# Optimization experiments

Measured on AMD Instinct MI355X. Metric: run time of the kernel, lower is better.

Reference implementation:

```python
import jax, jax.numpy as jnp
import numpy as np

N = 50000      # nodes
E = 800000     # edges
G = 64         # graphs in batch
H = 256        # hidden_channels
CE = 128       # coord embed dim = H//2
OTH = 6        # in_channels - 3
ED = 8         # edge_dim
EE = 128       # edge_embedding_dim
GD = 16        # global_dim
L = 3          # num_layers


def setup_inputs() -> dict:
    key = jax.random.key(0)
    ks = jax.random.split(key, 24)
    s = 0.05
    inp = {
        "x": jax.random.normal(ks[0], (N, 9), jnp.float32),
        "edge_index": jax.random.randint(ks[1], (2, E), 0, N),
        "batch": jnp.sort(jax.random.randint(ks[2], (N,), 0, G)),
        "edge_attr": jax.random.normal(ks[3], (E, ED), jnp.float32),
        "global_x": jax.random.normal(ks[4], (G, GD), jnp.float32),
        # coordinate embedder (Linear 3->128 + relu)
        "coord_W": jax.random.normal(ks[5], (3, CE), jnp.float32) * s,
        "coord_b": jnp.zeros((CE,), jnp.float32),
        # node_mlp (Linear 6->128 + relu)
        "node_W": jax.random.normal(ks[6], (OTH, CE), jnp.float32) * s,
        "node_b": jnp.zeros((CE,), jnp.float32),
        # edge processor (Linear 8->128 + relu) and projection 128->256
        "edge_W": jax.random.normal(ks[7], (ED, EE), jnp.float32) * s,
        "edge_b": jnp.zeros((EE,), jnp.float32),
        "proj_W": jax.random.normal(ks[8], (EE, H), jnp.float32) * s,
        "proj_b": jnp.zeros((H,), jnp.float32),
        # stacked GCN layer weights
        "gcn_W": jax.random.normal(ks[9], (L, H, H), jnp.float32) * s,
        "gcn_b": jnp.zeros((L, H), jnp.float32),
        # attention pooling
        "attn_w": jax.random.normal(ks[10], (H,), jnp.float32) * s,
        "attn_b": jnp.zeros((), jnp.float32),
        # global_mlp: Linear 16->256, relu, Linear 256->256
        "gmlp_W1": jax.random.normal(ks[11], (GD, H), jnp.float32) * s,
        "gmlp_b1": jnp.zeros((H,), jnp.float32),
        "gmlp_W2": jax.random.normal(ks[12], (H, H), jnp.float32) * s,
        "gmlp_b2": jnp.zeros((H,), jnp.float32),
        # fc_out: Linear 512->256, relu, Linear 256->1
        "fc_W1": jax.random.normal(ks[13], (2 * H, H), jnp.float32) * s,
        "fc_b1": jnp.zeros((H,), jnp.float32),
        "fc_W2": jax.random.normal(ks[14], (H, 1), jnp.float32) * s,
        "fc_b2": jnp.zeros((1,), jnp.float32),
    }
    return inp


def _segsum(v, idx, num):
    return jax.ops.segment_sum(v, idx, num_segments=num)


def reference(x, edge_index, batch, edge_attr, global_x,
              coord_W, coord_b, node_W, node_b, edge_W, edge_b,
              proj_W, proj_b, gcn_W, gcn_b, attn_w, attn_b,
              gmlp_W1, gmlp_b1, gmlp_W2, gmlp_b2,
              fc_W1, fc_b1, fc_W2, fc_b2):
    relu = jax.nn.relu
    # --- node embedding: coords + other features ---
    coord_emb = relu(x[:, :3] @ coord_W + coord_b)          # [N, 128]
    other_emb = relu(x[:, 3:] @ node_W + node_b)            # [N, 128]
    x_emb = jnp.concatenate([coord_emb, other_emb], axis=1)  # [N, 256]

    # --- edge embedding, aggregated to target nodes (index_add over col) ---
    edge_emb = relu(edge_attr @ edge_W + edge_b) @ proj_W + proj_b  # [E, 256]
    col0 = edge_index[1]
    node_msg = _segsum(edge_emb, col0, N)                    # [N, 256]

    # --- GCN normalization with self-loops ---
    sl = jnp.arange(N)
    row = jnp.concatenate([edge_index[0], sl])
    col = jnp.concatenate([edge_index[1], sl])
    deg = _segsum(jnp.ones_like(col, jnp.float32), col, N)   # >= 1
    dnorm = jax.lax.rsqrt(deg)
    efac = (dnorm[row] * dnorm[col])[:, None]                # [E+N, 1]

    # --- stacked GCN layers (edge messages re-added each layer, per source) ---
    for i in range(L):
        x_in = x_emb + node_msg
        h = x_in @ gcn_W[i]                                  # [N, 256]
        x_emb = _segsum(h[row] * efac, col, N) + gcn_b[i]
        if i < L - 1:
            x_emb = relu(x_emb)

    # --- attention pooling (per-graph softmax over batch index) ---
    scores = x_emb @ attn_w + attn_b                         # [N]
    m = jax.ops.segment_max(scores, batch, num_segments=G)
    e = jnp.exp(scores - m[batch])
    denom = _segsum(e, batch, G)
    attn = e / denom[batch]
    graph_emb = _segsum(x_emb * attn[:, None], batch, G)     # [G, 256]

    # --- global features + head ---
    g = relu(global_x @ gmlp_W1 + gmlp_b1) @ gmlp_W2 + gmlp_b2
    hcat = jnp.concatenate([graph_emb, g], axis=-1)          # [G, 512]
    out = relu(hcat @ fc_W1 + fc_b1) @ fc_W2 + fc_b2         # [G, 1]
    return out
```

## Files before the change

kernel.cpp:

```cpp
#include <hip/hip_runtime.h>


typedef float f32x4 __attribute__((ext_vector_type(4)));
typedef short s16x8 __attribute__((ext_vector_type(8)));

__device__ __forceinline__ unsigned short f2bf(float f) {
  union { float f; unsigned u; } v{f};
  unsigned r = v.u + 0x7fff + ((v.u >> 16) & 1);
  return (unsigned short)(r >> 16);
}
__device__ __forceinline__ float bf2f(unsigned short s) {
  union { unsigned u; float f; } v{(unsigned)s << 16};
  return v.f;
}
__device__ __forceinline__ float blo(unsigned u) {
  union { unsigned x; float f; } v{u << 16};
  return v.f;
}
__device__ __forceinline__ float bhi(unsigned u) {
  union { unsigned x; float f; } v{u & 0xffff0000u};
  return v.f;
}
__device__ __forceinline__ unsigned pk2(float a, float b) {
  return (unsigned)f2bf(a) | ((unsigned)f2bf(b) << 16);
}

__global__ void node_embed_kernel(const float* __restrict__ x,
                                  const float* __restrict__ coord_W, const float* __restrict__ coord_b,
                                  const float* __restrict__ node_W, const float* __restrict__ node_b,
                                  short* __restrict__ x0, int N) {
  int tid = threadIdx.x;
  int node = blockIdx.x * 8 + (tid >> 5);
  if (node >= N) return;
  int ch0 = (tid & 31) * 8;
  const float* xr = x + (size_t)node * 9;
  float a[8];
  if (ch0 < 128) {
    float4 b0 = *(const float4*)&coord_b[ch0];
    float4 b1 = *(const float4*)&coord_b[ch0 + 4];
    a[0]=b0.x; a[1]=b0.y; a[2]=b0.z; a[3]=b0.w; a[4]=b1.x; a[5]=b1.y; a[6]=b1.z; a[7]=b1.w;
#pragma unroll
    for (int k = 0; k < 3; k++) {
      float xv = xr[k];
      float4 w0 = *(const float4*)&coord_W[k * 128 + ch0];
      float4 w1 = *(const float4*)&coord_W[k * 128 + ch0 + 4];
      a[0] = fmaf(xv, w0.x, a[0]); a[1] = fmaf(xv, w0.y, a[1]);
      a[2] = fmaf(xv, w0.z, a[2]); a[3] = fmaf(xv, w0.w, a[3]);
      a[4] = fmaf(xv, w1.x, a[4]); a[5] = fmaf(xv, w1.y, a[5]);
      a[6] = fmaf(xv, w1.z, a[6]); a[7] = fmaf(xv, w1.w, a[7]);
    }
  } else {
    int c0 = ch0 - 128;
    float4 b0 = *(const float4*)&node_b[c0];
    float4 b1 = *(const float4*)&node_b[c0 + 4];
    a[0]=b0.x; a[1]=b0.y; a[2]=b0.z; a[3]=b0.w; a[4]=b1.x; a[5]=b1.y; a[6]=b1.z; a[7]=b1.w;
#pragma unroll
    for (int k = 0; k < 6; k++) {
      float xv = xr[3 + k];
      float4 w0 = *(const float4*)&node_W[k * 128 + c0];
      float4 w1 = *(const float4*)&node_W[k * 128 + c0 + 4];
      a[0] = fmaf(xv, w0.x, a[0]); a[1] = fmaf(xv, w0.y, a[1]);
      a[2] = fmaf(xv, w0.z, a[2]); a[3] = fmaf(xv, w0.w, a[3]);
      a[4] = fmaf(xv, w1.x, a[4]); a[5] = fmaf(xv, w1.y, a[5]);
      a[6] = fmaf(xv, w1.z, a[6]); a[7] = fmaf(xv, w1.w, a[7]);
    }
  }
  uint4 o;
  o.x = pk2(fmaxf(a[0], 0.f), fmaxf(a[1], 0.f));
  o.y = pk2(fmaxf(a[2], 0.f), fmaxf(a[3], 0.f));
  o.z = pk2(fmaxf(a[4], 0.f), fmaxf(a[5], 0.f));
  o.w = pk2(fmaxf(a[6], 0.f), fmaxf(a[7], 0.f));
  *(uint4*)&x0[(size_t)node * 256 + ch0] = o;
}

__global__ void count_kernel(const int* __restrict__ col, int* __restrict__ cnt, int E) {
  int e = blockIdx.x * 256 + threadIdx.x;
  if (e < E) atomicAdd(&cnt[col[e]], 1);
}

__global__ void breduce_kernel(const int* __restrict__ cnt, int* __restrict__ partials, int N) {
  __shared__ int red[256];
  int t = threadIdx.x;
  int i = blockIdx.x * 256 + t;
  int v = (i < N) ? cnt[i] : 0;
  red[t] = v;
  __syncthreads();
  for (int off = 128; off; off >>= 1) {
    if (t < off) red[t] += red[t + off];
    __syncthreads();
  }
  if (t == 0) partials[blockIdx.x] = red[0];
}

__global__ void scan_partials_kernel(int* __restrict__ partials, int nb) {
  __shared__ int s[1024];
  int t = threadIdx.x;
  for (int i = t; i < nb; i += 256) s[i] = partials[i];
  __syncthreads();
  if (t == 0) {
    int run = 0;
    for (int i = 0; i < nb; i++) { int c = s[i]; s[i] = run; run += c; }
  }
  __syncthreads();
  for (int i = t; i < nb; i += 256) partials[i] = s[i];
}

__global__ void scan_apply_kernel(const int* __restrict__ cnt, const int* __restrict__ partials,
                                  int* __restrict__ rowstart, float* __restrict__ dnorm,
                                  int* __restrict__ cursor, int N) {
  __shared__ int red[256];
  int t = threadIdx.x;
  int i = blockIdx.x * 256 + t;
  int v = (i < N) ? cnt[i] : 0;
  red[t] = v;
  __syncthreads();
  for (int off = 1; off < 256; off <<= 1) {
    int x = (t >= off) ? red[t - off] : 0;
    __syncthreads();
    red[t] += x;
    __syncthreads();
  }
  if (i < N) {
    int ex = red[t] - v + partials[blockIdx.x];
    rowstart[i] = ex;
    dnorm[i] = rsqrtf((float)(v + 1));
    cursor[i] = 0;
    if (i == N - 1) rowstart[N] = ex + v;
  }
}

__global__ void scatter_kernel(const int* __restrict__ row, const int* __restrict__ col,
                               const int* __restrict__ rowstart, int* __restrict__ cursor,
                               const float* __restrict__ dnorm,
                               int4* __restrict__ pk, int E) {
  int e = blockIdx.x * 256 + threadIdx.x;
  if (e >= E) return;
  int c = col[e], r = row[e];
  int p = atomicAdd(&cursor[c], 1);
  int slot = rowstart[c] + p;
  pk[slot] = make_int4(e, r, __float_as_int(dnorm[r] * dnorm[c]), 0);
}

__global__ void wt_kernel(const float* __restrict__ gcn_W, const float* __restrict__ proj_W,
                          short* __restrict__ gcnWt, short* __restrict__ projWt) {
  int idx = blockIdx.x * 256 + threadIdx.x;
  if (idx < 3 * 65536) {
    int l = idx >> 16, r = idx & 65535, n = r >> 8, k = r & 255;
    gcnWt[idx] = (short)f2bf(gcn_W[l * 65536 + k * 256 + n]);
  } else {
    int j = idx - 3 * 65536;
    int n = j >> 7, k = j & 127;
    projWt[j] = (short)f2bf(proj_W[k * 256 + n]);
  }
}

__global__ void edge_msg_kernel(const float* __restrict__ edge_attr,
                                const int4* __restrict__ pk,
                                const int* __restrict__ rowstart,
                                const float* __restrict__ edge_W, const float* __restrict__ edge_b,
                                short* __restrict__ msg128, int N) {
  int node = blockIdx.x;
  int ch = threadIdx.x;
  __shared__ float sW[8 * 128];
  __shared__ float sb[128];
  for (int i = ch; i < 8 * 128; i += 128) sW[i] = edge_W[i];
  sb[ch] = edge_b[ch];
  __syncthreads();
  float acc = 0.f;
  int s0 = rowstart[node], s1 = rowstart[node + 1];
  for (int s = s0; s < s1; s++) {
    int eid = pk[s].x;
    const float4* ea = (const float4*)(edge_attr + (size_t)eid * 8);
    float4 e0 = ea[0], e1 = ea[1];
    float t = sb[ch];
    t = fmaf(e0.x, sW[0 * 128 + ch], t);
    t = fmaf(e0.y, sW[1 * 128 + ch], t);
    t = fmaf(e0.z, sW[2 * 128 + ch], t);
    t = fmaf(e0.w, sW[3 * 128 + ch], t);
    t = fmaf(e1.x, sW[4 * 128 + ch], t);
    t = fmaf(e1.y, sW[5 * 128 + ch], t);
    t = fmaf(e1.z, sW[6 * 128 + ch], t);
    t = fmaf(e1.w, sW[7 * 128 + ch], t);
    acc += fmaxf(t, 0.f);
  }
  msg128[(size_t)node * 128 + ch] = (short)f2bf(acc);
}

__global__ void __launch_bounds__(256) fused_proj_gemm(
    const short* __restrict__ msg128, const short* __restrict__ projWt,
    const float* __restrict__ proj_b, const int* __restrict__ cnt,
    const short* __restrict__ x0, const short* __restrict__ W0t,
    short* __restrict__ node_msg, short* __restrict__ hout, int N) {
  __shared__ short As[64][136];
  __shared__ short Xs[64][264];
  int tid = threadIdx.x;
  int n0 = blockIdx.x * 64;
  for (int i = tid; i < 64 * 32; i += 256) {
    int r = i >> 5, c4 = (i & 31) << 2;
    int n = n0 + r;
    uint2 v = make_uint2(0, 0);
    if (n < N) v = *(const uint2*)&msg128[(size_t)n * 128 + c4];
    *(uint2*)&As[r][c4] = v;
  }
  __syncthreads();
  int wave = tid >> 6, lane = tid & 63;
  int mrow = wave * 16 + (lane & 15);
  int kgrp = (lane >> 4) * 8;
  f32x4 acc[16];
#pragma unroll
  for (int i = 0; i < 16; i++) acc[i] = (f32x4){0.f, 0.f, 0.f, 0.f};
  {
    const short* wbase = projWt + (size_t)(lane & 15) * 128 + kgrp;
#pragma unroll
    for (int kk = 0; kk < 4; kk++) {
      s16x8 a = *(const s16x8*)&As[mrow][kk * 32 + kgrp];
#pragma unroll
      for (int nf = 0; nf < 16; nf++) {
        s16x8 b = *(const s16x8*)&wbase[(size_t)nf * 16 * 128 + kk * 32];
        acc[nf] = __builtin_amdgcn_mfma_f32_16x16x32_bf16(a, b, acc[nf], 0, 0, 0);
      }
    }
  }
  int orow0 = wave * 16 + (lane >> 4) * 4;
  int ocol = lane & 15;
#pragma unroll
  for (int r = 0; r < 4; r++) {
    int i = orow0 + r;
    int n = n0 + i;
    if (n < N) {
      float cn = (float)cnt[n];
#pragma unroll
      for (int nf = 0; nf < 16; nf++) {
        int c = nf * 16 + ocol;
        float v = acc[nf][r] + cn * proj_b[c];
        unsigned short nm = f2bf(v);
        node_msg[(size_t)n * 256 + c] = (short)nm;
        Xs[i][c] = (short)f2bf(bf2f(nm) + bf2f((unsigned short)x0[(size_t)n * 256 + c]));
      }
    } else {
#pragma unroll
      for (int nf = 0; nf < 16; nf++) Xs[i][nf * 16 + ocol] = 0;
    }
  }
  __syncthreads();
#pragma unroll
  for (int i = 0; i < 16; i++) acc[i] = (f32x4){0.f, 0.f, 0.f, 0.f};
  {
    const short* wbase = W0t + (size_t)(lane & 15) * 256 + kgrp;
#pragma unroll
    for (int kk = 0; kk < 8; kk++) {
      s16x8 a = *(const s16x8*)&Xs[mrow][kk * 32 + kgrp];
#pragma unroll
      for (int nf = 0; nf < 16; nf++) {
        s16x8 b = *(const s16x8*)&wbase[(size_t)nf * 16 * 256 + kk * 32];
        acc[nf] = __builtin_amdgcn_mfma_f32_16x16x32_bf16(a, b, acc[nf], 0, 0, 0);
      }
    }
  }
#pragma unroll
  for (int nf = 0; nf < 16; nf++) {
#pragma unroll
    for (int r = 0; r < 4; r++) {
      int n = n0 + orow0 + r;
      if (n < N) hout[(size_t)n * 256 + nf * 16 + ocol] = (short)f2bf(acc[nf][r]);
    }
  }
}

__global__ void __launch_bounds__(256) gcn_agg_kernel(
    const short* __restrict__ h, const int4* __restrict__ pk,
    const int* __restrict__ rowstart, const float* __restrict__ dnorm,
    const float* __restrict__ b, const short* __restrict__ node_msg,
    short* __restrict__ xin, int N) {
  int lane = threadIdx.x & 63;
  int node = blockIdx.x * 4 + (threadIdx.x >> 6);
  if (node >= N) return;
  int ch0 = lane << 2;
  size_t rowb = (size_t)node * 256 + ch0;
  float dn = dnorm[node];
  float wgt = dn * dn;
  uint2 hv = *(const uint2*)&h[rowb];
  float a0 = blo(hv.x) * wgt, a1 = bhi(hv.x) * wgt;
  float a2 = blo(hv.y) * wgt, a3 = bhi(hv.y) * wgt;
  int s = rowstart[node], s1 = rowstart[node + 1];
  for (; s + 4 <= s1; s += 4) {
    int4 p0 = pk[s], p1 = pk[s + 1], p2 = pk[s + 2], p3 = pk[s + 3];
    float f0 = __int_as_float(p0.z), f1 = __int_as_float(p1.z);
    float f2 = __int_as_float(p2.z), f3 = __int_as_float(p3.z);
    uint2 v0 = *(const uint2*)&h[(size_t)p0.y * 256 + ch0];
    uint2 v1 = *(const uint2*)&h[(size_t)p1.y * 256 + ch0];
    uint2 v2 = *(const uint2*)&h[(size_t)p2.y * 256 + ch0];
    uint2 v3 = *(const uint2*)&h[(size_t)p3.y * 256 + ch0];
    a0 = fmaf(blo(v0.x), f0, a0); a1 = fmaf(bhi(v0.x), f0, a1);
    a2 = fmaf(blo(v0.y), f0, a2); a3 = fmaf(bhi(v0.y), f0, a3);
    a0 = fmaf(blo(v1.x), f1, a0); a1 = fmaf(bhi(v1.x), f1, a1);
    a2 = fmaf(blo(v1.y), f1, a2); a3 = fmaf(bhi(v1.y), f1, a3);
    a0 = fmaf(blo(v2.x), f2, a0); a1 = fmaf(bhi(v2.x), f2, a1);
    a2 = fmaf(blo(v2.y), f2, a2); a3 = fmaf(bhi(v2.y), f2, a3);
    a0 = fmaf(blo(v3.x), f3, a0); a1 = fmaf(bhi(v3.x), f3, a1);
    a2 = fmaf(blo(v3.y), f3, a2); a3 = fmaf(bhi(v3.y), f3, a3);
  }
  for (; s < s1; s++) {
    int4 p = pk[s];
    float f = __int_as_float(p.z);
    uint2 v = *(const uint2*)&h[(size_t)p.y * 256 + ch0];
    a0 = fmaf(blo(v.x), f, a0); a1 = fmaf(bhi(v.x), f, a1);
    a2 = fmaf(blo(v.y), f, a2); a3 = fmaf(bhi(v.y), f, a3);
  }
  float4 bv = *(const float4*)&b[ch0];
  uint2 mv = *(const uint2*)&node_msg[rowb];
  float y0 = fmaxf(a0 + bv.x, 0.f) + blo(mv.x);
  float y1 = fmaxf(a1 + bv.y, 0.f) + bhi(mv.x);
  float y2 = fmaxf(a2 + bv.z, 0.f) + blo(mv.y);
  float y3 = fmaxf(a3 + bv.w, 0.f) + bhi(mv.y);
  uint2 o;
  o.x = pk2(y0, y1);
  o.y = pk2(y2, y3);
  *(uint2*)&xin[rowb] = o;
}

__global__ void __launch_bounds__(256) gcn_gemm_mfma(
    const short* __restrict__ Xin, const short* __restrict__ Wt,
    short* __restrict__ Hout, int N) {
  __shared__ short As[64][264];
  int tid = threadIdx.x;
  int n0 = blockIdx.x * 64;
  for (int i = tid; i < 64 * 64; i += 256) {
    int r = i >> 6, c4 = (i & 63) << 2;
    int n = n0 + r;
    uint2 v = make_uint2(0, 0);
    if (n < N) v = *(const uint2*)&Xin[(size_t)n * 256 + c4];
    *(uint2*)&As[r][c4] = v;
  }
  __syncthreads();
  int wave = tid >> 6, lane = tid & 63;
  int mrow = wave * 16 + (lane & 15);
  int kgrp = (lane >> 4) * 8;
  f32x4 acc[16];
#pragma unroll
  for (int i = 0; i < 16; i++) acc[i] = (f32x4){0.f, 0.f, 0.f, 0.f};
  const short* wbase = Wt + (size_t)(lane & 15) * 256 + kgrp;
#pragma unroll
  for (int kk = 0; kk < 8; kk++) {
    s16x8 a = *(const s16x8*)&As[mrow][kk * 32 + kgrp];
#pragma unroll
    for (int nf = 0; nf < 16; nf++) {
      s16x8 b = *(const s16x8*)&wbase[(size_t)nf * 16 * 256 + kk * 32];
      acc[nf] = __builtin_amdgcn_mfma_f32_16x16x32_bf16(a, b, acc[nf], 0, 0, 0);
    }
  }
  int orow0 = wave * 16 + (lane >> 4) * 4;
  int ocol = lane & 15;
#pragma unroll
  for (int nf = 0; nf < 16; nf++) {
#pragma unroll
    for (int r = 0; r < 4; r++) {
      int n = n0 + orow0 + r;
      if (n < N) Hout[(size_t)n * 256 + nf * 16 + ocol] = (short)f2bf(acc[nf][r]);
    }
  }
}

__global__ void __launch_bounds__(256) final_agg_kernel(
    const short* __restrict__ h, const int4* __restrict__ pk,
    const int* __restrict__ rowstart, const float* __restrict__ dnorm,
    const float* __restrict__ b, short* __restrict__ x_emb,
    const float* __restrict__ attn_w, const float* __restrict__ attn_b,
    float* __restrict__ scores, int N) {
  int lane = threadIdx.x & 63;
  int node = blockIdx.x * 4 + (threadIdx.x >> 6);
  if (node >= N) return;
  int ch0 = lane << 2;
  size_t rowb = (size_t)node * 256 + ch0;
  float dn = dnorm[node];
  float wgt = dn * dn;
  uint2 hv = *(const uint2*)&h[rowb];
  float a0 = blo(hv.x) * wgt, a1 = bhi(hv.x) * wgt;
  float a2 = blo(hv.y) * wgt, a3 = bhi(hv.y) * wgt;
  int s = rowstart[node], s1 = rowstart[node + 1];
  for (; s + 4 <= s1; s += 4) {
    int4 p0 = pk[s], p1 = pk[s + 1], p2 = pk[s + 2], p3 = pk[s + 3];
    float f0 = __int_as_float(p0.z), f1 = __int_as_float(p1.z);
    float f2 = __int_as_float(p2.z), f3 = __int_as_float(p3.z);
    uint2 v0 = *(const uint2*)&h[(size_t)p0.y * 256 + ch0];
    uint2 v1 = *(const uint2*)&h[(size_t)p1.y * 256 + ch0];
    uint2 v2 = *(const uint2*)&h[(size_t)p2.y * 256 + ch0];
    uint2 v3 = *(const uint2*)&h[(size_t)p3.y * 256 + ch0];
    a0 = fmaf(blo(v0.x), f0, a0); a1 = fmaf(bhi(v0.x), f0, a1);
    a2 = fmaf(blo(v0.y), f0, a2); a3 = fmaf(bhi(v0.y), f0, a3);
    a0 = fmaf(blo(v1.x), f1, a0); a1 = fmaf(bhi(v1.x), f1, a1);
    a2 = fmaf(blo(v1.y), f1, a2); a3 = fmaf(bhi(v1.y), f1, a3);
    a0 = fmaf(blo(v2.x), f2, a0); a1 = fmaf(bhi(v2.x), f2, a1);
    a2 = fmaf(blo(v2.y), f2, a2); a3 = fmaf(bhi(v2.y), f2, a3);
    a0 = fmaf(blo(v3.x), f3, a0); a1 = fmaf(bhi(v3.x), f3, a1);
    a2 = fmaf(blo(v3.y), f3, a2); a3 = fmaf(bhi(v3.y), f3, a3);
  }
  for (; s < s1; s++) {
    int4 p = pk[s];
    float f = __int_as_float(p.z);
    uint2 v = *(const uint2*)&h[(size_t)p.y * 256 + ch0];
    a0 = fmaf(blo(v.x), f, a0); a1 = fmaf(bhi(v.x), f, a1);
    a2 = fmaf(blo(v.y), f, a2); a3 = fmaf(bhi(v.y), f, a3);
  }
  float4 bv = *(const float4*)&b[ch0];
  a0 += bv.x; a1 += bv.y; a2 += bv.z; a3 += bv.w;
  uint2 o;
  o.x = pk2(a0, a1);
  o.y = pk2(a2, a3);
  *(uint2*)&x_emb[rowb] = o;
  float4 aw = *(const float4*)&attn_w[ch0];
  float p = a0 * aw.x + a1 * aw.y + a2 * aw.z + a3 * aw.w;
#pragma unroll
  for (int off = 32; off; off >>= 1) p += __shfl_down(p, off);
  if (lane == 0) scores[node] = p + attn_b[0];
}

__global__ void gse_kernel(const int* __restrict__ batch, int* __restrict__ gs,
                           int* __restrict__ ge, int N) {
  int i = blockIdx.x * 256 + threadIdx.x;
  if (i >= N) return;
  int g = batch[i];
  if (i == 0) gs[g] = 0;
  else {
    int gp = batch[i - 1];
    if (gp != g) { gs[g] = i; ge[gp] = i - 1; }
  }
  if (i == N - 1) ge[g] = N - 1;
}

__global__ void softmax_kernel(const float* __restrict__ scores, const int* __restrict__ gs,
                               const int* __restrict__ ge, float* __restrict__ wnode) {
  int g = blockIdx.x;
  int tid = threadIdx.x;
  __shared__ float red[256];
  int s0 = gs[g], e1 = ge[g];
  if (s0 > e1) return;
  int s1 = e1 + 1;
  float m = -1e30f;
  for (int i = s0 + tid; i < s1; i += 256) m = fmaxf(m, scores[i]);
  red[tid] = m;
  __syncthreads();
  for (int off = 128; off; off >>= 1) {
    if (tid < off) red[tid] = fmaxf(red[tid], red[tid + off]);
    __syncthreads();
  }
  m = red[0];
  __syncthreads();
  float d = 0.f;
  for (int i = s0 + tid; i < s1; i += 256) d += expf(scores[i] - m);
  red[tid] = d;
  __syncthreads();
  for (int off = 128; off; off >>= 1) {
    if (tid < off) red[tid] += red[tid + off];
    __syncthreads();
  }
  float rd = 1.f / red[0];
  for (int i = s0 + tid; i < s1; i += 256) wnode[i] = expf(scores[i] - m) * rd;
}

__global__ void __launch_bounds__(256) pool_sum_kernel(
    const short* __restrict__ x_emb, const float* __restrict__ wnode,
    const int* __restrict__ batch, float* __restrict__ graph_emb, int N) {
  __shared__ int sb[256];
  __shared__ float sw[256];
  int ch = threadIdx.x;
  int i0 = blockIdx.x * 256;
  int lim = min(256, N - i0);
  if (ch < lim) { sb[ch] = batch[i0 + ch]; sw[ch] = wnode[i0 + ch]; }
  __syncthreads();
  int curg = sb[0];
  float acc = 0.f;
  for (int j = 0; j < lim; j++) {
    int g = sb[j];
    if (g != curg) {
      atomicAdd(&graph_emb[(size_t)curg * 256 + ch], acc);
      acc = 0.f;
      curg = g;
    }
    acc = fmaf(bf2f((unsigned short)x_emb[(size_t)(i0 + j) * 256 + ch]), sw[j], acc);
  }
  atomicAdd(&graph_emb[(size_t)curg * 256 + ch], acc);
}

__global__ void head_kernel(const float* __restrict__ global_x, const float* __restrict__ graph_emb,
                            const float* __restrict__ W1, const float* __restrict__ b1,
                            const float* __restrict__ W2, const float* __restrict__ b2,
                            const float* __restrict__ fW1, const float* __restrict__ fb1,
                            const float* __restrict__ fW2, const float* __restrict__ fb2,
                            float* __restrict__ out) {
  int g = blockIdx.x;
  int ch = threadIdx.x;
  __shared__ float t1[256], g2s[256], t3s[256];
  float a = b1[ch];
  const float* gx = global_x + g * 16;
#pragma unroll
  for (int k = 0; k < 16; k++) a = fmaf(gx[k], W1[k * 256 + ch], a);
  t1[ch] = fmaxf(a, 0.f);
  __syncthreads();
  float bb = b2[ch];
  for (int k = 0; k < 256; k++) bb = fmaf(t1[k], W2[k * 256 + ch], bb);
  g2s[ch] = bb;
  __syncthreads();
  float c = fb1[ch];
  const float* ger = graph_emb + (size_t)g * 256;
  for (int k = 0; k < 256; k++) c = fmaf(ger[k], fW1[k * 256 + ch], c);
  for (int k = 0; k < 256; k++) c = fmaf(g2s[k], fW1[(256 + k) * 256 + ch], c);
  t3s[ch] = fmaxf(c, 0.f);
  __syncthreads();
  t1[ch] = t3s[ch] * fW2[ch];
  __syncthreads();
  for (int off = 128; off; off >>= 1) {
    if (ch < off) t1[ch] += t1[ch + off];
    __syncthreads();
  }
  if (ch == 0) out[g] = t1[0] + fb2[0];
}

extern "C" void kernel_launch(void* const* d_in, const int* in_sizes, int n_in,
                              void* d_out, int out_size, void* d_ws, size_t ws_size,
                              hipStream_t stream) {
  const float* x        = (const float*)d_in[0];
  const int*   ei       = (const int*)d_in[1];
  const int*   batch    = (const int*)d_in[2];
  const float* edge_attr= (const float*)d_in[3];
  const float* global_x = (const float*)d_in[4];
  const float* coord_W  = (const float*)d_in[5];
  const float* coord_b  = (const float*)d_in[6];
  const float* node_W   = (const float*)d_in[7];
  const float* node_b   = (const float*)d_in[8];
  const float* edge_W   = (const float*)d_in[9];
  const float* edge_b   = (const float*)d_in[10];
  const float* proj_W   = (const float*)d_in[11];
  const float* proj_b   = (const float*)d_in[12];
  const float* gcn_W    = (const float*)d_in[13];
  const float* gcn_b    = (const float*)d_in[14];
  const float* attn_w   = (const float*)d_in[15];
  const float* attn_b   = (const float*)d_in[16];
  const float* gmlp_W1  = (const float*)d_in[17];
  const float* gmlp_b1  = (const float*)d_in[18];
  const float* gmlp_W2  = (const float*)d_in[19];
  const float* gmlp_b2  = (const float*)d_in[20];
  const float* fc_W1    = (const float*)d_in[21];
  const float* fc_b1    = (const float*)d_in[22];
  const float* fc_W2    = (const float*)d_in[23];
  const float* fc_b2    = (const float*)d_in[24];

  const int N = in_sizes[0] / 9;
  const int E = in_sizes[3] / 8;
  const int G = in_sizes[4] / 16;
  const int NB = (N + 255) / 256;

  char* w = (char*)d_ws;
  auto alloc = [&](size_t bytes) -> char* {
    char* p = w;
    w += (bytes + 255) & ~(size_t)255;
    return p;
  };
  short* x0       = (short*)alloc((size_t)N * 256 * 2);
  short* node_msg = (short*)alloc((size_t)N * 256 * 2);
  short* hA       = (short*)alloc((size_t)N * 256 * 2);
  short* hB       = (short*)alloc((size_t)N * 256 * 2);
  short* xinBuf   = (short*)alloc((size_t)N * 256 * 2);
  short* x_emb    = (short*)alloc((size_t)N * 256 * 2);
  short* msg128   = x_emb;
  int4*  pk       = (int4*)alloc((size_t)E * 16);
  short* gcnWt    = (short*)alloc((size_t)3 * 65536 * 2);
  short* projWt   = (short*)alloc((size_t)256 * 128 * 2);
  int*   cnt      = (int*)alloc((size_t)N * 4);
  int*   rowstart = (int*)alloc((size_t)(N + 1) * 4);
  int*   cursor   = (int*)alloc((size_t)N * 4);
  float* dnorm    = (float*)alloc((size_t)N * 4);
  float* scores   = (float*)alloc((size_t)N * 4);
  float* wnode    = (float*)alloc((size_t)N * 4);
  int*   partials = (int*)alloc((size_t)NB * 4);
  int*   gs       = (int*)alloc((size_t)G * 4);
  int*   ge       = (int*)alloc((size_t)G * 4);
  float* graph_emb= (float*)alloc((size_t)G * 256 * 4);

  hipMemsetAsync(cnt, 0, (size_t)N * 4, stream);
  hipMemsetAsync(gs, 0x7f, (size_t)G * 4, stream);
  hipMemsetAsync(ge, 0xff, (size_t)G * 4, stream);
  hipMemsetAsync(graph_emb, 0, (size_t)G * 256 * 4, stream);

  wt_kernel<<<(3 * 65536 + 256 * 128 + 255) / 256, 256, 0, stream>>>(gcn_W, proj_W, gcnWt, projWt);
  node_embed_kernel<<<(N + 7) / 8, 256, 0, stream>>>(
      x, coord_W, coord_b, node_W, node_b, x0, N);
  count_kernel<<<(E + 255) / 256, 256, 0, stream>>>(ei + E, cnt, E);
  breduce_kernel<<<NB, 256, 0, stream>>>(cnt, partials, N);
  scan_partials_kernel<<<1, 256, 0, stream>>>(partials, NB);
  scan_apply_kernel<<<NB, 256, 0, stream>>>(cnt, partials, rowstart, dnorm, cursor, N);
  scatter_kernel<<<(E + 255) / 256, 256, 0, stream>>>(
      ei, ei + E, rowstart, cursor, dnorm, pk, E);
  edge_msg_kernel<<<N, 128, 0, stream>>>(edge_attr, pk, rowstart, edge_W, edge_b, msg128, N);
  fused_proj_gemm<<<(N + 63) / 64, 256, 0, stream>>>(
      msg128, projWt, proj_b, cnt, x0, gcnWt, node_msg, hA, N);
  gcn_agg_kernel<<<(N + 3) / 4, 256, 0, stream>>>(
      hA, pk, rowstart, dnorm, gcn_b, node_msg, xinBuf, N);
  gcn_gemm_mfma<<<(N + 63) / 64, 256, 0, stream>>>(
      xinBuf, gcnWt + 65536, hB, N);
  gcn_agg_kernel<<<(N + 3) / 4, 256, 0, stream>>>(
      hB, pk, rowstart, dnorm, gcn_b + 256, node_msg, xinBuf, N);
  gcn_gemm_mfma<<<(N + 63) / 64, 256, 0, stream>>>(
      xinBuf, gcnWt + 2 * 65536, hA, N);
  final_agg_kernel<<<(N + 3) / 4, 256, 0, stream>>>(
      hA, pk, rowstart, dnorm, gcn_b + 512, x_emb, attn_w, attn_b, scores, N);
  gse_kernel<<<(N + 255) / 256, 256, 0, stream>>>(batch, gs, ge, N);
  softmax_kernel<<<G, 256, 0, stream>>>(scores, gs, ge, wnode);
  pool_sum_kernel<<<NB, 256, 0, stream>>>(x_emb, wnode, batch, graph_emb, N);
  head_kernel<<<G, 256, 0, stream>>>(global_x, graph_emb, gmlp_W1, gmlp_b1, gmlp_W2, gmlp_b2,
                                     fc_W1, fc_b1, fc_W2, fc_b2, (float*)d_out);
}
```

Measured before the change: 928.3 us.

## Split CSR edge records, rewrite edge MLP kernel, unfuse proj and first GEMM

```diff
diff --git a/kernel.cpp b/kernel.cpp
--- a/kernel.cpp
+++ b/kernel.cpp
@@ -132,13 +132,14 @@
 __global__ void scatter_kernel(const int* __restrict__ row, const int* __restrict__ col,
                                const int* __restrict__ rowstart, int* __restrict__ cursor,
                                const float* __restrict__ dnorm,
-                               int4* __restrict__ pk, int E) {
+                               int2* __restrict__ pk8, int* __restrict__ eids, int E) {
   int e = blockIdx.x * 256 + threadIdx.x;
   if (e >= E) return;
   int c = col[e], r = row[e];
   int p = atomicAdd(&cursor[c], 1);
   int slot = rowstart[c] + p;
-  pk[slot] = make_int4(e, r, __float_as_int(dnorm[r] * dnorm[c]), 0);
+  pk8[slot] = make_int2(r, __float_as_int(dnorm[r] * dnorm[c]));
+  eids[slot] = e;
 }
 
 __global__ void wt_kernel(const float* __restrict__ gcn_W, const float* __restrict__ proj_W,
@@ -154,45 +155,63 @@
   }
 }
 
-__global__ void edge_msg_kernel(const float* __restrict__ edge_attr,
-                                const int4* __restrict__ pk,
-                                const int* __restrict__ rowstart,
-                                const float* __restrict__ edge_W, const float* __restrict__ edge_b,
-                                short* __restrict__ msg128, int N) {
-  int node = blockIdx.x;
-  int ch = threadIdx.x;
-  __shared__ float sW[8 * 128];
-  __shared__ float sb[128];
-  for (int i = ch; i < 8 * 128; i += 128) sW[i] = edge_W[i];
-  sb[ch] = edge_b[ch];
-  __syncthreads();
-  float acc = 0.f;
-  int s0 = rowstart[node], s1 = rowstart[node + 1];
-  for (int s = s0; s < s1; s++) {
-    int eid = pk[s].x;
-    const float4* ea = (const float4*)(edge_attr + (size_t)eid * 8);
-    float4 e0 = ea[0], e1 = ea[1];
-    float t = sb[ch];
-    t = fmaf(e0.x, sW[0 * 128 + ch], t);
-    t = fmaf(e0.y, sW[1 * 128 + ch], t);
-    t = fmaf(e0.z, sW[2 * 128 + ch], t);
-    t = fmaf(e0.w, sW[3 * 128 + ch], t);
-    t = fmaf(e1.x, sW[4 * 128 + ch], t);
-    t = fmaf(e1.y, sW[5 * 128 + ch], t);
-    t = fmaf(e1.z, sW[6 * 128 + ch], t);
-    t = fmaf(e1.w, sW[7 * 128 + ch], t);
-    acc += fmaxf(t, 0.f);
-  }
-  msg128[(size_t)node * 128 + ch] = (short)f2bf(acc);
-}
-
-__global__ void __launch_bounds__(256) fused_proj_gemm(
+__global__ void __launch_bounds__(256) edge_msg_kernel(
+    const float* __restrict__ edge_attr, const int* __restrict__ eids,
+    const int* __restrict__ rowstart,
+    const float* __restrict__ edge_W, const float* __restrict__ edge_b,
+    unsigned* __restrict__ msg128u, int N) {
+  int lane = threadIdx.x & 63;
+  int node = blockIdx.x * 4 + (threadIdx.x >> 6);
+  if (node >= N) return;
+  int ch0 = lane * 2;
+  float wa[8], wb[8];
+#pragma unroll
+  for (int k = 0; k < 8; k++) {
+    float2 w = *(const float2*)&edge_W[k * 128 + ch0];
+    wa[k] = w.x; wb[k] = w.y;
+  }
+  float2 bb = *(const float2*)&edge_b[ch0];
+  float acc0 = 0.f, acc1 = 0.f;
+  int s = rowstart[node], s1 = rowstart[node + 1];
+  const float4* ea4 = (const float4*)edge_attr;
+  for (; s + 4 <= s1; s += 4) {
+    int e0 = eids[s], e1 = eids[s + 1], e2 = eids[s + 2], e3 = eids[s + 3];
+    float4 a00 = ea4[(size_t)e0 * 2], a01 = ea4[(size_t)e0 * 2 + 1];
+    float4 a10 = ea4[(size_t)e1 * 2], a11 = ea4[(size_t)e1 * 2 + 1];
+    float4 a20 = ea4[(size_t)e2 * 2], a21 = ea4[(size_t)e2 * 2 + 1];
+    float4 a30 = ea4[(size_t)e3 * 2], a31 = ea4[(size_t)e3 * 2 + 1];
+    float t0, t1;
+#define EMLP(lo, hi)                                                        \
+    t0 = bb.x; t1 = bb.y;                                                   \
+    t0 = fmaf(lo.x, wa[0], t0); t1 = fmaf(lo.x, wb[0], t1);                 \
+    t0 = fmaf(lo.y, wa[1], t0); t1 = fmaf(lo.y, wb[1], t1);                 \
+    t0 = fmaf(lo.z, wa[2], t0); t1 = fmaf(lo.z, wb[2], t1);                 \
+    t0 = fmaf(lo.w, wa[3], t0); t1 = fmaf(lo.w, wb[3], t1);                 \
+    t0 = fmaf(hi.x, wa[4], t0); t1 = fmaf(hi.x, wb[4], t1);                 \
+    t0 = fmaf(hi.y, wa[5], t0); t1 = fmaf(hi.y, wb[5], t1);                 \
+    t0 = fmaf(hi.z, wa[6], t0); t1 = fmaf(hi.z, wb[6], t1);                 \
+    t0 = fmaf(hi.w, wa[7], t0); t1 = fmaf(hi.w, wb[7], t1);                 \
+    acc0 += fmaxf(t0, 0.f); acc1 += fmaxf(t1, 0.f);
+    EMLP(a00, a01)
+    EMLP(a10, a11)
+    EMLP(a20, a21)
+    EMLP(a30, a31)
+  }
+  for (; s < s1; s++) {
+    int e = eids[s];
+    float4 lo = ea4[(size_t)e * 2], hi = ea4[(size_t)e * 2 + 1];
+    float t0, t1;
+    EMLP(lo, hi)
+  }
+#undef EMLP
+  msg128u[(size_t)node * 64 + lane] = pk2(acc0, acc1);
+}
+
+__global__ void __launch_bounds__(256) proj_gemm_mfma(
     const short* __restrict__ msg128, const short* __restrict__ projWt,
     const float* __restrict__ proj_b, const int* __restrict__ cnt,
-    const short* __restrict__ x0, const short* __restrict__ W0t,
-    short* __restrict__ node_msg, short* __restrict__ hout, int N) {
+    short* __restrict__ node_msg, int N) {
   __shared__ short As[64][136];
-  __shared__ short Xs[64][264];
   int tid = threadIdx.x;
   int n0 = blockIdx.x * 64;
   for (int i = tid; i < 64 * 32; i += 256) {
@@ -209,66 +228,81 @@
   f32x4 acc[16];
 #pragma unroll
   for (int i = 0; i < 16; i++) acc[i] = (f32x4){0.f, 0.f, 0.f, 0.f};
-  {
-    const short* wbase = projWt + (size_t)(lane & 15) * 128 + kgrp;
-#pragma unroll
-    for (int kk = 0; kk < 4; kk++) {
-      s16x8 a = *(const s16x8*)&As[mrow][kk * 32 + kgrp];
-#pragma unroll
-      for (int nf = 0; nf < 16; nf++) {
-        s16x8 b = *(const s16x8*)&wbase[(size_t)nf * 16 * 128 + kk * 32];
-        acc[nf] = __builtin_amdgcn_mfma_f32_16x16x32_bf16(a, b, acc[nf], 0, 0, 0);
-      }
+  const short* wbase = projWt + (size_t)(lane & 15) * 128 + kgrp;
+#pragma unroll
+  for (int kk = 0; kk < 4; kk++) {
+    s16x8 a = *(const s16x8*)&As[mrow][kk * 32 + kgrp];
+#pragma unroll
+    for (int nf = 0; nf < 16; nf++) {
+      s16x8 b = *(const s16x8*)&wbase[(size_t)nf * 16 * 128 + kk * 32];
+      acc[nf] = __builtin_amdgcn_mfma_f32_16x16x32_bf16(a, b, acc[nf], 0, 0, 0);
     }
   }
   int orow0 = wave * 16 + (lane >> 4) * 4;
   int ocol = lane & 15;
 #pragma unroll
   for (int r = 0; r < 4; r++) {
-    int i = orow0 + r;
-    int n = n0 + i;
+    int n = n0 + orow0 + r;
     if (n < N) {
       float cn = (float)cnt[n];
 #pragma unroll
       for (int nf = 0; nf < 16; nf++) {
         int c = nf * 16 + ocol;
-        float v = acc[nf][r] + cn * proj_b[c];
-        unsigned short nm = f2bf(v);
-        node_msg[(size_t)n * 256 + c] = (short)nm;
-        Xs[i][c] = (short)f2bf(bf2f(nm) + bf2f((unsigned short)x0[(size_t)n * 256 + c]));
+        node_msg[(size_t)n * 256 + c] = (short)f2bf(acc[nf][r] + cn * proj_b[c]);
       }
-    } else {
-#pragma unroll
-      for (int nf = 0; nf < 16; nf++) Xs[i][nf * 16 + ocol] = 0;
-    }
-  }
-  __syncthreads();
+    }
+  }
+}
+
+__global__ void __launch_bounds__(256) gcn_gemm_add_mfma(
+    const short* __restrict__ X, const short* __restrict__ M,
+    const short* __restrict__ Wt, short* __restrict__ Hout, int N) {
+  __shared__ short As[64][264];
+  int tid = threadIdx.x;
+  int n0 = blockIdx.x * 64;
+  for (int i = tid; i < 64 * 64; i += 256) {
+    int r = i >> 6, c4 = (i & 63) << 2;
+    int n = n0 + r;
+    uint2 o = make_uint2(0, 0);
+    if (n < N) {
+      uint2 xv = *(const uint2*)&X[(size_t)n * 256 + c4];
+      uint2 mv = *(const uint2*)&M[(size_t)n * 256 + c4];
+      o.x = pk2(blo(xv.x) + blo(mv.x), bhi(xv.x) + bhi(mv.x));
+      o.y = pk2(blo(xv.y) + blo(mv.y), bhi(xv.y) + bhi(mv.y));
+    }
+    *(uint2*)&As[r][c4] = o;
+  }
+  __syncthreads();
+  int wave = tid >> 6, lane = tid & 63;
+  int mrow = wave * 16 + (lane & 15);
+  int kgrp = (lane >> 4) * 8;
+  f32x4 acc[16];
 #pragma unroll
   for (int i = 0; i < 16; i++) acc[i] = (f32x4){0.f, 0.f, 0.f, 0.f};
-  {
-    const short* wbase = W0t + (size_t)(lane & 15) * 256 + kgrp;
-#pragma unroll
-    for (int kk = 0; kk < 8; kk++) {
-      s16x8 a = *(const s16x8*)&Xs[mrow][kk * 32 + kgrp];
-#pragma unroll
-      for (int nf = 0; nf < 16; nf++) {
-        s16x8 b = *(const s16x8*)&wbase[(size_t)nf * 16 * 256 + kk * 32];
-        acc[nf] = __builtin_amdgcn_mfma_f32_16x16x32_bf16(a, b, acc[nf], 0, 0, 0);
-      }
-    }
-  }
+  const short* wbase = Wt + (size_t)(lane & 15) * 256 + kgrp;
+#pragma unroll
+  for (int kk = 0; kk < 8; kk++) {
+    s16x8 a = *(const s16x8*)&As[mrow][kk * 32 + kgrp];
+#pragma unroll
+    for (int nf = 0; nf < 16; nf++) {
+      s16x8 b = *(const s16x8*)&wbase[(size_t)nf * 16 * 256 + kk * 32];
+      acc[nf] = __builtin_amdgcn_mfma_f32_16x16x32_bf16(a, b, acc[nf], 0, 0, 0);
+    }
+  }
+  int orow0 = wave * 16 + (lane >> 4) * 4;
+  int ocol = lane & 15;
 #pragma unroll
   for (int nf = 0; nf < 16; nf++) {
 #pragma unroll
     for (int r = 0; r < 4; r++) {
       int n = n0 + orow0 + r;
-      if (n < N) hout[(size_t)n * 256 + nf * 16 + ocol] = (short)f2bf(acc[nf][r]);
+      if (n < N) Hout[(size_t)n * 256 + nf * 16 + ocol] = (short)f2bf(acc[nf][r]);
     }
   }
 }
 
 __global__ void __launch_bounds__(256) gcn_agg_kernel(
-    const short* __restrict__ h, const int4* __restrict__ pk,
+    const short* __restrict__ h, const int2* __restrict__ pk8,
     const int* __restrict__ rowstart, const float* __restrict__ dnorm,
     const float* __restrict__ b, const short* __restrict__ node_msg,
     short* __restrict__ xin, int N) {
@@ -284,13 +318,13 @@
   float a2 = blo(hv.y) * wgt, a3 = bhi(hv.y) * wgt;
   int s = rowstart[node], s1 = rowstart[node + 1];
   for (; s + 4 <= s1; s += 4) {
-    int4 p0 = pk[s], p1 = pk[s + 1], p2 = pk[s + 2], p3 = pk[s + 3];
-    float f0 = __int_as_float(p0.z), f1 = __int_as_float(p1.z);
-    float f2 = __int_as_float(p2.z), f3 = __int_as_float(p3.z);
-    uint2 v0 = *(const uint2*)&h[(size_t)p0.y * 256 + ch0];
-    uint2 v1 = *(const uint2*)&h[(size_t)p1.y * 256 + ch0];
-    uint2 v2 = *(const uint2*)&h[(size_t)p2.y * 256 + ch0];
-    uint2 v3 = *(const uint2*)&h[(size_t)p3.y * 256 + ch0];
+    int2 p0 = pk8[s], p1 = pk8[s + 1], p2 = pk8[s + 2], p3 = pk8[s + 3];
+    float f0 = __int_as_float(p0.y), f1 = __int_as_float(p1.y);
+    float f2 = __int_as_float(p2.y), f3 = __int_as_float(p3.y);
+    uint2 v0 = *(const uint2*)&h[(size_t)p0.x * 256 + ch0];
+    uint2 v1 = *(const uint2*)&h[(size_t)p1.x * 256 + ch0];
+    uint2 v2 = *(const uint2*)&h[(size_t)p2.x * 256 + ch0];
+    uint2 v3 = *(const uint2*)&h[(size_t)p3.x * 256 + ch0];
     a0 = fmaf(blo(v0.x), f0, a0); a1 = fmaf(bhi(v0.x), f0, a1);
     a2 = fmaf(blo(v0.y), f0, a2); a3 = fmaf(bhi(v0.y), f0, a3);
     a0 = fmaf(blo(v1.x), f1, a0); a1 = fmaf(bhi(v1.x), f1, a1);
@@ -301,9 +335,9 @@
     a2 = fmaf(blo(v3.y), f3, a2); a3 = fmaf(bhi(v3.y), f3, a3);
   }
   for (; s < s1; s++) {
-    int4 p = pk[s];
-    float f = __int_as_float(p.z);
-    uint2 v = *(const uint2*)&h[(size_t)p.y * 256 + ch0];
+    int2 p = pk8[s];
+    float f = __int_as_float(p.y);
+    uint2 v = *(const uint2*)&h[(size_t)p.x * 256 + ch0];
     a0 = fmaf(blo(v.x), f, a0); a1 = fmaf(bhi(v.x), f, a1);
     a2 = fmaf(blo(v.y), f, a2); a3 = fmaf(bhi(v.y), f, a3);
   }
@@ -362,7 +396,7 @@
 }
 
 __global__ void __launch_bounds__(256) final_agg_kernel(
-    const short* __restrict__ h, const int4* __restrict__ pk,
+    const short* __restrict__ h, const int2* __restrict__ pk8,
     const int* __restrict__ rowstart, const float* __restrict__ dnorm,
     const float* __restrict__ b, short* __restrict__ x_emb,
     const float* __restrict__ attn_w, const float* __restrict__ attn_b,
@@ -379,13 +413,13 @@
   float a2 = blo(hv.y) * wgt, a3 = bhi(hv.y) * wgt;
   int s = rowstart[node], s1 = rowstart[node + 1];
   for (; s + 4 <= s1; s += 4) {
-    int4 p0 = pk[s], p1 = pk[s + 1], p2 = pk[s + 2], p3 = pk[s + 3];
-    float f0 = __int_as_float(p0.z), f1 = __int_as_float(p1.z);
-    float f2 = __int_as_float(p2.z), f3 = __int_as_float(p3.z);
-    uint2 v0 = *(const uint2*)&h[(size_t)p0.y * 256 + ch0];
-    uint2 v1 = *(const uint2*)&h[(size_t)p1.y * 256 + ch0];
-    uint2 v2 = *(const uint2*)&h[(size_t)p2.y * 256 + ch0];
-    uint2 v3 = *(const uint2*)&h[(size_t)p3.y * 256 + ch0];
+    int2 p0 = pk8[s], p1 = pk8[s + 1], p2 = pk8[s + 2], p3 = pk8[s + 3];
+    float f0 = __int_as_float(p0.y), f1 = __int_as_float(p1.y);
+    float f2 = __int_as_float(p2.y), f3 = __int_as_float(p3.y);
+    uint2 v0 = *(const uint2*)&h[(size_t)p0.x * 256 + ch0];
+    uint2 v1 = *(const uint2*)&h[(size_t)p1.x * 256 + ch0];
+    uint2 v2 = *(const uint2*)&h[(size_t)p2.x * 256 + ch0];
+    uint2 v3 = *(const uint2*)&h[(size_t)p3.x * 256 + ch0];
     a0 = fmaf(blo(v0.x), f0, a0); a1 = fmaf(bhi(v0.x), f0, a1);
     a2 = fmaf(blo(v0.y), f0, a2); a3 = fmaf(bhi(v0.y), f0, a3);
     a0 = fmaf(blo(v1.x), f1, a0); a1 = fmaf(bhi(v1.x), f1, a1);
@@ -396,9 +430,9 @@
     a2 = fmaf(blo(v3.y), f3, a2); a3 = fmaf(bhi(v3.y), f3, a3);
   }
   for (; s < s1; s++) {
-    int4 p = pk[s];
-    float f = __int_as_float(p.z);
-    uint2 v = *(const uint2*)&h[(size_t)p.y * 256 + ch0];
+    int2 p = pk8[s];
+    float f = __int_as_float(p.y);
+    uint2 v = *(const uint2*)&h[(size_t)p.x * 256 + ch0];
     a0 = fmaf(blo(v.x), f, a0); a1 = fmaf(bhi(v.x), f, a1);
     a2 = fmaf(blo(v.y), f, a2); a3 = fmaf(bhi(v.y), f, a3);
   }
@@ -563,7 +597,8 @@
   short* xinBuf   = (short*)alloc((size_t)N * 256 * 2);
   short* x_emb    = (short*)alloc((size_t)N * 256 * 2);
   short* msg128   = x_emb;
-  int4*  pk       = (int4*)alloc((size_t)E * 16);
+  int2*  pk8      = (int2*)alloc((size_t)E * 8);
+  int*   eids     = (int*)alloc((size_t)E * 4);
   short* gcnWt    = (short*)alloc((size_t)3 * 65536 * 2);
   short* projWt   = (short*)alloc((size_t)256 * 128 * 2);
   int*   cnt      = (int*)alloc((size_t)N * 4);
@@ -590,20 +625,23 @@
   scan_partials_kernel<<<1, 256, 0, stream>>>(partials, NB);
   scan_apply_kernel<<<NB, 256, 0, stream>>>(cnt, partials, rowstart, dnorm, cursor, N);
   scatter_kernel<<<(E + 255) / 256, 256, 0, stream>>>(
-      ei, ei + E, rowstart, cursor, dnorm, pk, E);
-  edge_msg_kernel<<<N, 128, 0, stream>>>(edge_attr, pk, rowstart, edge_W, edge_b, msg128, N);
-  fused_proj_gemm<<<(N + 63) / 64, 256, 0, stream>>>(
-      msg128, projWt, proj_b, cnt, x0, gcnWt, node_msg, hA, N);
+      ei, ei + E, rowstart, cursor, dnorm, pk8, eids, E);
+  edge_msg_kernel<<<(N + 3) / 4, 256, 0, stream>>>(
+      edge_attr, eids, rowstart, edge_W, edge_b, (unsigned*)msg128, N);
+  proj_gemm_mfma<<<(N + 63) / 64, 256, 0, stream>>>(
+      msg128, projWt, proj_b, cnt, node_msg, N);
+  gcn_gemm_add_mfma<<<(N + 63) / 64, 256, 0, stream>>>(
+      x0, node_msg, gcnWt, hA, N);
   gcn_agg_kernel<<<(N + 3) / 4, 256, 0, stream>>>(
-      hA, pk, rowstart, dnorm, gcn_b, node_msg, xinBuf, N);
+      hA, pk8, rowstart, dnorm, gcn_b, node_msg, xinBuf, N);
   gcn_gemm_mfma<<<(N + 63) / 64, 256, 0, stream>>>(
       xinBuf, gcnWt + 65536, hB, N);
   gcn_agg_kernel<<<(N + 3) / 4, 256, 0, stream>>>(
-      hB, pk, rowstart, dnorm, gcn_b + 256, node_msg, xinBuf, N);
+      hB, pk8, rowstart, dnorm, gcn_b + 256, node_msg, xinBuf, N);
   gcn_gemm_mfma<<<(N + 63) / 64, 256, 0, stream>>>(
       xinBuf, gcnWt + 2 * 65536, hA, N);
   final_agg_kernel<<<(N + 3) / 4, 256, 0, stream>>>(
-      hA, pk, rowstart, dnorm, gcn_b + 512, x_emb, attn_w, attn_b, scores, N);
+      hA, pk8, rowstart, dnorm, gcn_b + 512, x_emb, attn_w, attn_b, scores, N);
   gse_kernel<<<(N + 255) / 256, 256, 0, stream>>>(batch, gs, ge, N);
   softmax_kernel<<<G, 256, 0, stream>>>(scores, gs, ge, wnode);
   pool_sum_kernel<<<NB, 256, 0, stream>>>(x_emb, wnode, batch, graph_emb, N);
```

After: 923.4 us. No clear change (-0.5%).
